# Kernel tuning notes

Measured on AMD Instinct MI355X. Metric: run time of the kernel, lower is better.

## Reference

```python
import jax, jax.numpy as jnp
import numpy as np
from jax import lax

ITERS = 10
EPS = 1e-6
LOSS_WEIGHT = 1.0


def _max_pool3x3(x):
    # F.max_pool2d(x, kernel_size=3, stride=1, padding=1): torch pads with -inf for max pool
    return lax.reduce_window(x, -jnp.inf, lax.max,
                             window_dimensions=(1, 1, 3, 3),
                             window_strides=(1, 1, 1, 1),
                             padding=((0, 0), (0, 0), (1, 1), (1, 1)))


def _soft_erode(x):
    return -_max_pool3x3(-x)


def _soft_dilate(x):
    return _max_pool3x3(x)


def _soft_open(x):
    return _soft_dilate(_soft_erode(x))


def _soft_skel(img, iters):
    img = jnp.clip(img, 0.0, 1.0)
    img1 = _soft_open(img)
    skel = jax.nn.relu(img - img1)
    for _ in range(iters):
        img = _soft_erode(img)
        img1 = _soft_open(img)
        delta = jax.nn.relu(img - img1)
        skel = skel + jax.nn.relu(delta - skel * delta)
    return skel


def setup_inputs() -> dict:
    key = jax.random.key(0)
    k1, k2 = jax.random.split(key)
    B, C, H, W = 8, 2, 1024, 1024
    pred = jax.random.normal(k1, (B, C, H, W), dtype=jnp.float32)
    target = jax.random.uniform(k2, (B, C, H, W), dtype=jnp.float32)
    return {"pred": pred, "target": target}


def reference(pred, target):
    # sigmoid on logits
    p = jax.nn.sigmoid(pred)  # [B,C,H,W]
    t = target.astype(p.dtype)
    # per-class channel slicing is equivalent to channel-wise ops (pooling is per-channel)
    skel_p = _soft_skel(p, ITERS)
    skel_t = _soft_skel(t, ITERS)
    hw = (2, 3)
    tprec = jnp.sum(skel_p * t, axis=hw) / (jnp.sum(skel_p, axis=hw) + EPS)  # [B,C]
    tsens = jnp.sum(skel_t * p, axis=hw) / (jnp.sum(skel_t, axis=hw) + EPS)  # [B,C]
    cl_dice = 1.0 - 2.0 * tprec * tsens / (tprec + tsens + EPS)  # [B,C]
    # original: per-class mean over batch, then mean over classes == global mean
    return LOSS_WEIGHT * jnp.mean(cl_dice)
```

## Files before the change

### kernel.cpp

```cpp
#include <hip/hip_runtime.h>


#define TILE 64
#define HALO 12
#define RROWS 88
#define SD 52
#define IMG 1024
#define NBC 16
#define NITER 11
#define LEPS 1e-6f

typedef unsigned int u32;
typedef _Float16 hv2 __attribute__((ext_vector_type(2)));

struct __align__(16) U4 { u32 v[4]; };

__device__ __forceinline__ hv2 H2(u32 x) { union { u32 u; hv2 h; } c; c.u = x; return c.h; }
__device__ __forceinline__ u32 U2(hv2 x) { union { u32 u; hv2 h; } c; c.h = x; return c.u; }
__device__ __forceinline__ hv2 hmin2v(hv2 a, hv2 b) { return __builtin_elementwise_min(a, b); }
__device__ __forceinline__ hv2 hmax2v(hv2 a, hv2 b) { return __builtin_elementwise_max(a, b); }
__device__ __forceinline__ u32 dpp_prev16(u32 x) {
    return (u32)__builtin_amdgcn_update_dpp(0, (int)x, 0x101, 0xf, 0xf, true);
}
__device__ __forceinline__ u32 dpp_next16(u32 x) {
    return (u32)__builtin_amdgcn_update_dpp(0, (int)x, 0x111, 0xf, 0xf, true);
}
__device__ __forceinline__ u32 alignh(u32 hi, u32 lo) {
    return (u32)((((unsigned long long)hi << 32) | lo) >> 16);
}
__device__ __forceinline__ float sigmoidf(float x) { return 1.0f / (1.0f + __expf(-x)); }

template<bool IS_MIN>
__device__ __forceinline__ void hpass(const u32 d[4], u32 o[4]) {
    u32 dm = dpp_prev16(d[3]);
    u32 dp = dpp_next16(d[0]);
    u32 a[5];
    a[0] = alignh(d[0], dm);
    a[1] = alignh(d[1], d[0]);
    a[2] = alignh(d[2], d[1]);
    a[3] = alignh(d[3], d[2]);
    a[4] = alignh(dp,   d[3]);
#pragma unroll
    for (int q = 0; q < 4; ++q) {
        if (IS_MIN) o[q] = U2(hmin2v(hmin2v(H2(a[q]), H2(d[q])), H2(a[q + 1])));
        else        o[q] = U2(hmax2v(hmax2v(H2(a[q]), H2(d[q])), H2(a[q + 1])));
    }
}

template<int JMAX>
__device__ __forceinline__ void iter_body(int k, u32* cur, u32* oth,
        int strip, int g16, int coldw, bool wact, int rs_d,
        bool edgeI, int rdLo, int rdHi, bool edgeL, bool edgeR,
        hv2 (&Cv)[4][4])
{
    const int lo = min(k + 1, 11);
    const int hi = max(86 - k, 76);
    const int blk = (JMAX == 5) ? (((strip & 3) << 2) | (strip >> 2))
                                : ((strip & ~3) | ((strip & 1) << 1) | ((strip >> 1) & 1));
    const int rs_e = min(lo + JMAX * blk, hi - (JMAX - 1));
    {
        const u32* p = cur + (rs_e - 1) * SD + coldw;
        u32* qo = oth + rs_e * SD + coldw;
        U4 r0, r1, r2;
        *(uint4*)r0.v = *(const uint4*)(p);
        *(uint4*)r1.v = *(const uint4*)(p + SD);
#pragma unroll
        for (int j = 0; j < JMAX; ++j) {
            *(uint4*)r2.v = *(const uint4*)(p + (j + 2) * SD);
            U4 vv, o;
#pragma unroll
            for (int q = 0; q < 4; ++q)
                vv.v[q] = U2(hmin2v(hmin2v(H2(r0.v[q]), H2(r1.v[q])), H2(r2.v[q])));
            hpass<true>(vv.v, o.v);
            if (wact) *(uint4*)(qo + j * SD) = *(const uint4*)o.v;
            r0 = r1; r1 = r2;
        }
    }
    __syncthreads();

    {
        U4 w[6];
        if (edgeI) {
            const u32* p = oth + (rs_d - 1) * SD + coldw;
#pragma unroll
            for (int j = 0; j < 6; ++j)
                *(uint4*)w[j].v = *(const uint4*)(p + j * SD);
        } else {
#pragma unroll
            for (int j = 0; j < 6; ++j) {
                int rr = min(max(rs_d - 1 + j, rdLo), rdHi);
                *(uint4*)w[j].v = *(const uint4*)(oth + rr * SD + coldw);
            }
        }
        U4 V[4], m[4];
#pragma unroll
        for (int i = 0; i < 4; ++i) {
#pragma unroll
            for (int q = 0; q < 4; ++q)
                V[i].v[q] = U2(hmax2v(hmax2v(H2(w[i].v[q]), H2(w[i + 1].v[q])),
                                      H2(w[i + 2].v[q])));
            hpass<false>(V[i].v, m[i].v);
        }

        if (edgeL && g16 == 1) {
#pragma unroll
            for (int i = 0; i < 4; ++i) {
                u32 d2 = V[i].v[2];
                u32 sw = (d2 >> 16) | (d2 << 16);
                u32 pm = U2(hmax2v(H2(d2), H2(sw)));
                m[i].v[2] = (m[i].v[2] & 0xFFFF0000u) | (pm & 0xFFFFu);
            }
        }
        if (edgeR && g16 == 9) {
#pragma unroll
            for (int i = 0; i < 4; ++i) {
                u32 d1 = V[i].v[1];
                u32 sw = (d1 >> 16) | (d1 << 16);
                u32 pm = U2(hmax2v(H2(d1), H2(sw)));
                m[i].v[1] = (m[i].v[1] & 0x0000FFFFu) | (pm & 0xFFFF0000u);
            }
        }

        const u32* pc = cur + rs_d * SD + coldw;
#pragma unroll
        for (int i = 0; i < 4; ++i) {
            U4 a; *(uint4*)a.v = *(const uint4*)(pc + i * SD);
#pragma unroll
            for (int qd = 0; qd < 4; ++qd) {
                hv2 D = H2(m[i].v[qd]);
                hv2 z; z[0] = (_Float16)0; z[1] = (_Float16)0;
                hv2 d = hmax2v(H2(a.v[qd]) - D, z);
                hv2 c = Cv[i][qd];
                Cv[i][qd] = c - c * d;
            }
        }
    }
    __syncthreads();
}

__global__ __launch_bounds__(256, 4)
void skel_tile_kernel(const float* __restrict__ pred,
                      const float* __restrict__ target,
                      float* __restrict__ ws)
{
    __shared__ __align__(16) u32 bufA[RROWS * SD];
    __shared__ __align__(16) u32 bufB[RROWS * SD];

    const int tid = threadIdx.x;
    const int bc  = blockIdx.z & (NBC - 1);
    const int img = blockIdx.z >> 4;
    const int r0  = blockIdx.y * TILE;
    const int c0  = blockIdx.x * TILE;

    const float* src = (img == 0) ? pred : target;
    const size_t base = (size_t)bc * (size_t)(IMG * IMG);

    const bool edgeT = (blockIdx.y == 0);
    const bool edgeB = (blockIdx.y == 15);
    const bool edgeL = (blockIdx.x == 0);
    const bool edgeR = (blockIdx.x == 15);
    const bool edgeI = !(edgeT || edgeB);
    const int rdLo = edgeT ? 12 : 0;
    const int rdHi = edgeB ? 75 : (RROWS - 1);

    for (int t = tid; t < 88 * 12; t += 256) {
        int rr = t / 12;
        int g  = t - rr * 12;
        int gr = min(max(r0 + rr - HALO, 0), IMG - 1);
        const float* rowp = src + base + (size_t)gr * IMG;
        float f[8];
        int gc0 = c0 + 8 * g - HALO;
        if (g <= 10 && gc0 >= 0 && gc0 + 8 <= IMG) {
            float4 v0 = *(const float4*)(rowp + gc0);
            float4 v1 = *(const float4*)(rowp + gc0 + 4);
            f[0] = v0.x; f[1] = v0.y; f[2] = v0.z; f[3] = v0.w;
            f[4] = v1.x; f[5] = v1.y; f[6] = v1.z; f[7] = v1.w;
        } else {
#pragma unroll
            for (int i = 0; i < 8; ++i) {
                int rc = min(8 * g + i, 87);
                int gc = min(max(c0 + rc - HALO, 0), IMG - 1);
                f[i] = rowp[gc];
            }
        }
        U4 u;
#pragma unroll
        for (int q = 0; q < 4; ++q) {
            float a = f[2 * q], b = f[2 * q + 1];
            if (img == 0) { a = sigmoidf(a); b = sigmoidf(b); }
            else { a = fminf(fmaxf(a, 0.f), 1.f); b = fminf(fmaxf(b, 0.f), 1.f); }
            hv2 p; p[0] = (_Float16)a; p[1] = (_Float16)b;
            u.v[q] = U2(p);
        }
        *(uint4*)&bufA[rr * SD + 4 * g] = *(const uint4*)u.v;
    }

    const int strip = tid >> 4;
    const int g16   = tid & 15;
    const int coldw = 4 * min(g16, 11);
    const bool wact = (g16 < 12);

    const int rs_d = 12 + 4 * strip;

    hv2 Cv[4][4];
#pragma unroll
    for (int j = 0; j < 4; ++j)
#pragma unroll
        for (int q = 0; q < 4; ++q) { Cv[j][q][0] = (_Float16)1; Cv[j][q][1] = (_Float16)1; }

    u32* cur = bufA;
    u32* oth = bufB;

    __syncthreads();

#pragma unroll 1
    for (int k = 0; k < 3; ++k) {
        iter_body<6>(k, cur, oth, strip, g16, coldw, wact, rs_d,
                     edgeI, rdLo, rdHi, edgeL, edgeR, Cv);
        u32* t_ = cur; cur = oth; oth = t_;
    }
#pragma unroll 1
    for (int k = 3; k < NITER; ++k) {
        iter_body<5>(k, cur, oth, strip, g16, coldw, wact, rs_d,
                     edgeI, rdLo, rdHi, edgeL, edgeR, Cv);
        u32* t_ = cur; cur = oth; oth = t_;
    }

    const float* osrc = (img == 0) ? target : pred;
    float s_sum = 0.0f, sp_sum = 0.0f;
#pragma unroll
    for (int j = 0; j < 4; ++j) {
        int orow = r0 + 4 * strip + j;
#pragma unroll
        for (int q = 0; q < 4; ++q) {
#pragma unroll
            for (int e = 0; e < 2; ++e) {
                int rc = 8 * g16 + 2 * q + e;
                if (rc >= 12 && rc <= 75) {
                    float sv = 1.0f - (float)Cv[j][q][e];
                    float ov = osrc[base + (size_t)orow * IMG + (c0 + rc - HALO)];
                    if (img == 1) ov = sigmoidf(ov);
                    s_sum  += sv;
                    sp_sum += sv * ov;
                }
            }
        }
    }

#pragma unroll
    for (int off = 32; off > 0; off >>= 1) {
        s_sum  += __shfl_down(s_sum,  off, 64);
        sp_sum += __shfl_down(sp_sum, off, 64);
    }
    float* red = (float*)bufA;
    if ((tid & 63) == 0) {
        red[(tid >> 6) * 2 + 0] = sp_sum;
        red[(tid >> 6) * 2 + 1] = s_sum;
    }
    __syncthreads();
    if (tid == 0) {
        float a = (red[0] + red[2]) + (red[4] + red[6]);
        float b = (red[1] + red[3]) + (red[5] + red[7]);
        float* acc = ws + (size_t)blockIdx.z * 2;
        atomicAdd(acc + 0, a);
        atomicAdd(acc + 1, b);
    }
}

__global__ void finalize_kernel(const float* __restrict__ ws, float* __restrict__ out)
{
    if (threadIdx.x == 0) {
        float acc = 0.0f;
        for (int bc = 0; bc < NBC; ++bc) {
            float spt = ws[(0 * NBC + bc) * 2 + 0];
            float sp  = ws[(0 * NBC + bc) * 2 + 1];
            float stp = ws[(1 * NBC + bc) * 2 + 0];
            float st  = ws[(1 * NBC + bc) * 2 + 1];
            float tprec = spt / (sp + LEPS);
            float tsens = stp / (st + LEPS);
            acc += 1.0f - 2.0f * tprec * tsens / (tprec + tsens + LEPS);
        }
        out[0] = acc / (float)NBC;
    }
}

extern "C" void kernel_launch(void* const* d_in, const int* in_sizes, int n_in,
                              void* d_out, int out_size, void* d_ws, size_t ws_size,
                              hipStream_t stream) {
    const float* pred   = (const float*)d_in[0];
    const float* target = (const float*)d_in[1];
    float* ws  = (float*)d_ws;
    float* out = (float*)d_out;

    hipMemsetAsync(d_ws, 0, 2 * NBC * 2 * sizeof(float), stream);

    dim3 grid(IMG / TILE, IMG / TILE, 2 * NBC);
    skel_tile_kernel<<<grid, 256, 0, stream>>>(pred, target, ws);
    finalize_kernel<<<1, 64, 0, stream>>>(ws, out);
}
```

Measured before the change: 482.9 us.

## Keep eroded rows in registers to fuse dilation and skip LDS re-reads

```diff
diff --git a/kernel.cpp b/kernel.cpp
--- a/kernel.cpp
+++ b/kernel.cpp
@@ -47,98 +47,20 @@
     }
 }
 
-template<int JMAX>
-__device__ __forceinline__ void iter_body(int k, u32* cur, u32* oth,
-        int strip, int g16, int coldw, bool wact, int rs_d,
-        bool edgeI, int rdLo, int rdHi, bool edgeL, bool edgeR,
-        hv2 (&Cv)[4][4])
-{
-    const int lo = min(k + 1, 11);
-    const int hi = max(86 - k, 76);
-    const int blk = (JMAX == 5) ? (((strip & 3) << 2) | (strip >> 2))
-                                : ((strip & ~3) | ((strip & 1) << 1) | ((strip >> 1) & 1));
-    const int rs_e = min(lo + JMAX * blk, hi - (JMAX - 1));
-    {
-        const u32* p = cur + (rs_e - 1) * SD + coldw;
-        u32* qo = oth + rs_e * SD + coldw;
-        U4 r0, r1, r2;
-        *(uint4*)r0.v = *(const uint4*)(p);
-        *(uint4*)r1.v = *(const uint4*)(p + SD);
-#pragma unroll
-        for (int j = 0; j < JMAX; ++j) {
-            *(uint4*)r2.v = *(const uint4*)(p + (j + 2) * SD);
-            U4 vv, o;
-#pragma unroll
-            for (int q = 0; q < 4; ++q)
-                vv.v[q] = U2(hmin2v(hmin2v(H2(r0.v[q]), H2(r1.v[q])), H2(r2.v[q])));
-            hpass<true>(vv.v, o.v);
-            if (wact) *(uint4*)(qo + j * SD) = *(const uint4*)o.v;
-            r0 = r1; r1 = r2;
-        }
-    }
-    __syncthreads();
-
-    {
-        U4 w[6];
-        if (edgeI) {
-            const u32* p = oth + (rs_d - 1) * SD + coldw;
-#pragma unroll
-            for (int j = 0; j < 6; ++j)
-                *(uint4*)w[j].v = *(const uint4*)(p + j * SD);
-        } else {
-#pragma unroll
-            for (int j = 0; j < 6; ++j) {
-                int rr = min(max(rs_d - 1 + j, rdLo), rdHi);
-                *(uint4*)w[j].v = *(const uint4*)(oth + rr * SD + coldw);
-            }
-        }
-        U4 V[4], m[4];
-#pragma unroll
-        for (int i = 0; i < 4; ++i) {
-#pragma unroll
-            for (int q = 0; q < 4; ++q)
-                V[i].v[q] = U2(hmax2v(hmax2v(H2(w[i].v[q]), H2(w[i + 1].v[q])),
-                                      H2(w[i + 2].v[q])));
-            hpass<false>(V[i].v, m[i].v);
-        }
-
-        if (edgeL && g16 == 1) {
-#pragma unroll
-            for (int i = 0; i < 4; ++i) {
-                u32 d2 = V[i].v[2];
-                u32 sw = (d2 >> 16) | (d2 << 16);
-                u32 pm = U2(hmax2v(H2(d2), H2(sw)));
-                m[i].v[2] = (m[i].v[2] & 0xFFFF0000u) | (pm & 0xFFFFu);
-            }
-        }
-        if (edgeR && g16 == 9) {
-#pragma unroll
-            for (int i = 0; i < 4; ++i) {
-                u32 d1 = V[i].v[1];
-                u32 sw = (d1 >> 16) | (d1 << 16);
-                u32 pm = U2(hmax2v(H2(d1), H2(sw)));
-                m[i].v[1] = (m[i].v[1] & 0x0000FFFFu) | (pm & 0xFFFF0000u);
-            }
-        }
-
-        const u32* pc = cur + rs_d * SD + coldw;
-#pragma unroll
-        for (int i = 0; i < 4; ++i) {
-            U4 a; *(uint4*)a.v = *(const uint4*)(pc + i * SD);
-#pragma unroll
-            for (int qd = 0; qd < 4; ++qd) {
-                hv2 D = H2(m[i].v[qd]);
-                hv2 z; z[0] = (_Float16)0; z[1] = (_Float16)0;
-                hv2 d = hmax2v(H2(a.v[qd]) - D, z);
-                hv2 c = Cv[i][qd];
-                Cv[i][qd] = c - c * d;
-            }
-        }
-    }
-    __syncthreads();
-}
-
-__global__ __launch_bounds__(256, 4)
+__device__ __forceinline__ void erode_row(const u32* cur, u32* oth, int r,
+                                          int coldw, bool wact) {
+    U4 a, b, c, vv, o;
+    *(uint4*)a.v = *(const uint4*)(cur + (r - 1) * SD + coldw);
+    *(uint4*)b.v = *(const uint4*)(cur + r * SD + coldw);
+    *(uint4*)c.v = *(const uint4*)(cur + (r + 1) * SD + coldw);
+#pragma unroll
+    for (int q = 0; q < 4; ++q)
+        vv.v[q] = U2(hmin2v(hmin2v(H2(a.v[q]), H2(b.v[q])), H2(c.v[q])));
+    hpass<true>(vv.v, o.v);
+    if (wact) *(uint4*)(oth + r * SD + coldw) = *(const uint4*)o.v;
+}
+
+__global__ __launch_bounds__(256, 3)
 void skel_tile_kernel(const float* __restrict__ pred,
                       const float* __restrict__ target,
                       float* __restrict__ ws)
@@ -159,9 +81,6 @@
     const bool edgeB = (blockIdx.y == 15);
     const bool edgeL = (blockIdx.x == 0);
     const bool edgeR = (blockIdx.x == 15);
-    const bool edgeI = !(edgeT || edgeB);
-    const int rdLo = edgeT ? 12 : 0;
-    const int rdHi = edgeB ? 75 : (RROWS - 1);
 
     for (int t = tid; t < 88 * 12; t += 256) {
         int rr = t / 12;
@@ -201,6 +120,7 @@
     const bool wact = (g16 < 12);
 
     const int rs_d = 12 + 4 * strip;
+    const int re0  = 11 + 4 * strip;
 
     hv2 Cv[4][4];
 #pragma unroll
@@ -213,17 +133,98 @@
 
     __syncthreads();
 
+    U4 ep[4];
+#pragma unroll
+    for (int i = 0; i < 4; ++i)
+        *(uint4*)ep[i].v = *(const uint4*)(cur + (rs_d + i) * SD + coldw);
+
 #pragma unroll 1
-    for (int k = 0; k < 3; ++k) {
-        iter_body<6>(k, cur, oth, strip, g16, coldw, wact, rs_d,
-                     edgeI, rdLo, rdHi, edgeL, edgeR, Cv);
-        u32* t_ = cur; cur = oth; oth = t_;
-    }
-#pragma unroll 1
-    for (int k = 3; k < NITER; ++k) {
-        iter_body<5>(k, cur, oth, strip, g16, coldw, wact, rs_d,
-                     edgeI, rdLo, rdHi, edgeL, edgeR, Cv);
-        u32* t_ = cur; cur = oth; oth = t_;
+    for (int k = 0; k < NITER; ++k) {
+        U4 e[6];
+        {
+            const u32* p = cur + (re0 - 1) * SD + coldw;
+            U4 r0v, r1v, r2v;
+            *(uint4*)r0v.v = *(const uint4*)(p);
+            *(uint4*)r1v.v = *(const uint4*)(p + SD);
+#pragma unroll
+            for (int j = 0; j < 6; ++j) {
+                *(uint4*)r2v.v = *(const uint4*)(p + (j + 2) * SD);
+                U4 vv;
+#pragma unroll
+                for (int q = 0; q < 4; ++q)
+                    vv.v[q] = U2(hmin2v(hmin2v(H2(r0v.v[q]), H2(r1v.v[q])), H2(r2v.v[q])));
+                hpass<true>(vv.v, e[j].v);
+                r0v = r1v; r1v = r2v;
+            }
+            u32* qo = oth + re0 * SD + coldw;
+            if (wact) {
+#pragma unroll
+                for (int j = 0; j < 4; ++j)
+                    *(uint4*)(qo + j * SD) = *(const uint4*)e[j].v;
+                if (strip == 15) {
+                    *(uint4*)(qo + 4 * SD) = *(const uint4*)e[4].v;
+                    *(uint4*)(qo + 5 * SD) = *(const uint4*)e[5].v;
+                }
+            }
+        }
+        {
+            const int nx = 10 - k;
+            if (strip < nx) {
+                erode_row(cur, oth, (k + 1) + strip, coldw, wact);
+                erode_row(cur, oth, (86 - k) - strip, coldw, wact);
+            }
+        }
+        __syncthreads();
+
+        {
+            U4 elo = e[0], ehi = e[5];
+            if (edgeT && strip == 0)  elo = e[1];
+            if (edgeB && strip == 15) ehi = e[4];
+            U4 V[4], m[4];
+#pragma unroll
+            for (int q = 0; q < 4; ++q) {
+                V[0].v[q] = U2(hmax2v(hmax2v(H2(elo.v[q]),  H2(e[1].v[q])), H2(e[2].v[q])));
+                V[1].v[q] = U2(hmax2v(hmax2v(H2(e[1].v[q]), H2(e[2].v[q])), H2(e[3].v[q])));
+                V[2].v[q] = U2(hmax2v(hmax2v(H2(e[2].v[q]), H2(e[3].v[q])), H2(e[4].v[q])));
+                V[3].v[q] = U2(hmax2v(hmax2v(H2(e[3].v[q]), H2(e[4].v[q])), H2(ehi.v[q])));
+            }
+#pragma unroll
+            for (int i = 0; i < 4; ++i) hpass<false>(V[i].v, m[i].v);
+
+            if (edgeL && g16 == 1) {
+#pragma unroll
+                for (int i = 0; i < 4; ++i) {
+                    u32 d2 = V[i].v[2];
+                    u32 sw = (d2 >> 16) | (d2 << 16);
+                    u32 pm = U2(hmax2v(H2(d2), H2(sw)));
+                    m[i].v[2] = (m[i].v[2] & 0xFFFF0000u) | (pm & 0xFFFFu);
+                }
+            }
+            if (edgeR && g16 == 9) {
+#pragma unroll
+                for (int i = 0; i < 4; ++i) {
+                    u32 d1 = V[i].v[1];
+                    u32 sw = (d1 >> 16) | (d1 << 16);
+                    u32 pm = U2(hmax2v(H2(d1), H2(sw)));
+                    m[i].v[1] = (m[i].v[1] & 0x0000FFFFu) | (pm & 0xFFFF0000u);
+                }
+            }
+
+#pragma unroll
+            for (int i = 0; i < 4; ++i) {
+#pragma unroll
+                for (int qd = 0; qd < 4; ++qd) {
+                    hv2 D = H2(m[i].v[qd]);
+                    hv2 z; z[0] = (_Float16)0; z[1] = (_Float16)0;
+                    hv2 d = hmax2v(H2(ep[i].v[qd]) - D, z);
+                    hv2 c = Cv[i][qd];
+                    Cv[i][qd] = c - c * d;
+                }
+                ep[i] = e[i + 1];
+            }
+        }
+
+        { u32* t_ = cur; cur = oth; oth = t_; }
     }
 
     const float* osrc = (img == 0) ? target : pred;
@@ -234,10 +235,10 @@
 #pragma unroll
         for (int q = 0; q < 4; ++q) {
 #pragma unroll
-            for (int e = 0; e < 2; ++e) {
-                int rc = 8 * g16 + 2 * q + e;
+            for (int e2 = 0; e2 < 2; ++e2) {
+                int rc = 8 * g16 + 2 * q + e2;
                 if (rc >= 12 && rc <= 75) {
-                    float sv = 1.0f - (float)Cv[j][q][e];
+                    float sv = 1.0f - (float)Cv[j][q][e2];
                     float ov = osrc[base + (size_t)orow * IMG + (c0 + rc - HALO)];
                     if (img == 1) ov = sigmoidf(ov);
                     s_sum  += sv;
```

Result: no change. 488.7 us (+1.2%).
